# Performance work log

Measured on AMD Instinct MI355X. Metric: run time of the kernel, lower is better.

Reference implementation:

```python
import jax, jax.numpy as jnp
import numpy as np

D_MODEL = 256
D_STATE = 64
D_CONV = 4
EXPAND = 2
HEADDIM = 64
D_INNER = EXPAND * D_MODEL            # 512
NHEADS = D_INNER // HEADDIM           # 8
D_XBC = D_INNER + 2 * D_STATE         # 640 (x, B, C; ngroups=1)
D_IN_PROJ = 2 * D_INNER + 2 * D_STATE + NHEADS  # 1160


def setup_inputs() -> dict:
    key = jax.random.key(0)
    ks = jax.random.split(key, 8)
    x = jax.random.normal(ks[0], (64, 5000, 12), jnp.float32)
    W_in = jax.random.normal(ks[1], (D_MODEL, D_IN_PROJ), jnp.float32) * 0.02
    conv_w = jax.random.normal(ks[2], (D_XBC, D_CONV), jnp.float32) * 0.1
    conv_b = jnp.zeros((D_XBC,), jnp.float32)
    A_log = jnp.log(jax.random.uniform(ks[3], (NHEADS,), jnp.float32, 1.0, 16.0))
    dt_bias = jax.random.normal(ks[4], (NHEADS,), jnp.float32) * 0.1
    D = jnp.ones((NHEADS,), jnp.float32)
    norm_w = jnp.ones((D_INNER,), jnp.float32)
    W_out = jax.random.normal(ks[5], (D_INNER, D_MODEL), jnp.float32) * 0.02
    return {"x": x, "W_in": W_in, "conv_w": conv_w, "conv_b": conv_b,
            "A_log": A_log, "dt_bias": dt_bias, "D": D,
            "norm_w": norm_w, "W_out": W_out}


def _mamba2(u, W_in, conv_w, conv_b, A_log, dt_bias, D, norm_w, W_out):
    b, l, _ = u.shape
    zxbcdt = u @ W_in                                   # (b,l,1160)
    z = zxbcdt[..., :D_INNER]                           # (b,l,512)
    xBC = zxbcdt[..., D_INNER:D_INNER + D_XBC]          # (b,l,640)
    dt = zxbcdt[..., D_INNER + D_XBC:]                  # (b,l,8)
    # causal depthwise conv1d (kernel 4) + SiLU
    xp = jnp.pad(xBC, ((0, 0), (D_CONV - 1, 0), (0, 0)))
    xBC = sum(xp[:, k:k + l, :] * conv_w[:, k] for k in range(D_CONV)) + conv_b
    xBC = jax.nn.silu(xBC)
    xs = xBC[..., :D_INNER].reshape(b, l, NHEADS, HEADDIM)
    Bm = xBC[..., D_INNER:D_INNER + D_STATE]            # (b,l,64)
    Cm = xBC[..., D_INNER + D_STATE:]                   # (b,l,64)
    dt = jax.nn.softplus(dt + dt_bias)                  # (b,l,h)
    A = -jnp.exp(A_log)                                 # (h,)

    def step(h, inp):
        x_t, dt_t, B_t, C_t = inp                       # (b,h,p),(b,h),(b,n),(b,n)
        decay = jnp.exp(dt_t * A)                       # (b,h)
        h = h * decay[..., None, None] + (dt_t[..., None] * x_t)[..., None] * B_t[:, None, None, :]
        y = jnp.einsum('bhpn,bn->bhp', h, C_t)
        return h, y

    h0 = jnp.zeros((b, NHEADS, HEADDIM, D_STATE), u.dtype)
    _, ys = jax.lax.scan(step, h0, (xs.transpose(1, 0, 2, 3), dt.transpose(1, 0, 2),
                                    Bm.transpose(1, 0, 2), Cm.transpose(1, 0, 2)))
    y = ys.transpose(1, 0, 2, 3) + D[None, None, :, None] * xs   # D skip, per head
    y = y.reshape(b, l, D_INNER)
    # RMSNormGated: gate then rmsnorm
    y = y * jax.nn.silu(z)
    y = y * jax.lax.rsqrt(jnp.mean(y * y, axis=-1, keepdims=True) + 1e-5) * norm_w
    return y @ W_out                                    # (b,l,256)


def reference(x, W_in, conv_w, conv_b, A_log, dt_bias, D, norm_w, W_out):
    b = x.shape[0]
    u = x.reshape(b, 250, 240)                          # 'b (t p1) f -> b t (p1 f)'
    u = jnp.pad(u, ((0, 0), (0, 0), (0, D_MODEL - 240)))
    y = _mamba2(u, W_in, conv_w, conv_b, A_log, dt_bias, D, norm_w, W_out)
    y = jax.nn.selu(y)                                  # AlphaDropout is identity at eval
    y = y[..., :240]
    return y.reshape(b, 5000, 12)
```

## Files before the change

kernel.cpp:

```cpp
#include <hip/hip_runtime.h>
#include <cstdint>
#include <cstddef>

#define D_MODEL 256
#define D_STATE 64
#define HEADDIM 64
#define D_INNER 512
#define NHEADS 8
#define D_XBC 640
#define NPROJ 1160
#define ZXW 1152
#define BATCH 64
#define SEQ 250
#define ROWS (BATCH * SEQ)
#define KIN 240
#define KPAD 256
#define NPAD 1280
#define TPAD 256

typedef __bf16 bf16x8 __attribute__((ext_vector_type(8)));
typedef float f32x4 __attribute__((ext_vector_type(4)));

typedef __attribute__((address_space(1))) const void gv_t;
typedef __attribute__((address_space(3))) void lv_t;

__device__ __forceinline__ float readlane_f(float v, int lane) {
    return __uint_as_float(__builtin_amdgcn_readlane(__float_as_uint(v), lane));
}
__device__ __forceinline__ float silu_f(float x) { return x * (1.f / (1.f + __expf(-x))); }
__device__ __forceinline__ unsigned short bf16_rne(float f) {
    unsigned int u = __float_as_uint(f);
    u += 0x7fff + ((u >> 16) & 1);
    return (unsigned short)(u >> 16);
}
__device__ __forceinline__ float bf2f(unsigned short u) {
    return __uint_as_float(((unsigned int)u) << 16);
}
__device__ __forceinline__ unsigned int pack2(float a, float b) {
    return (unsigned int)bf16_rne(a) | ((unsigned int)bf16_rne(b) << 16);
}

#define NA (ROWS * KPAD)
#define NB (NPAD * KPAD)
#define NW (D_MODEL * D_INNER)
__global__ __launch_bounds__(256) void cast_all_kernel(const float* __restrict__ x,
                                                       const float* __restrict__ Win,
                                                       const float* __restrict__ Wout,
                                                       unsigned short* __restrict__ a_bf,
                                                       unsigned short* __restrict__ bt_bf,
                                                       unsigned short* __restrict__ wt_bf) {
    int idx = blockIdx.x * 256 + threadIdx.x;
    if (idx < NA) {
        int row = idx >> 8, c = idx & 255;
        float v = (c < KIN) ? x[row * KIN + c] : 0.f;
        a_bf[idx] = bf16_rne(v);
    } else if (idx < NA + NB) {
        int r = idx - NA;
        int n = r >> 8, k = r & 255;
        float v = (n < NPROJ && k < KIN) ? Win[k * NPROJ + n] : 0.f;
        bt_bf[r] = bf16_rne(v);
    } else if (idx < NA + NB + NW) {
        int r = idx - NA - NB;
        int n = r & 255, k = r >> 8;
        wt_bf[n * D_INNER + k] = bf16_rne(Wout[k * D_MODEL + n]);
    }
}

__global__ __launch_bounds__(256) void gemm1_mfma(const unsigned short* __restrict__ A,
                                                  const unsigned short* __restrict__ Bt,
                                                  unsigned short* __restrict__ Czx,
                                                  float* __restrict__ dtraw) {
    __shared__ unsigned short As[128 * 32];
    __shared__ unsigned short Bs[128 * 32];
    const int tid = threadIdx.x;
    const int lane = tid & 63, wave = tid >> 6;
    const int wm = wave >> 1, wn = wave & 1;
    const int q = lane >> 4, l15 = lane & 15;
    const int rowBase = blockIdx.y * 128, colBase = blockIdx.x * 128;
    f32x4 acc[4][4] = {};

    const int sr = tid >> 2;
    const int sc = (tid & 3) * 8;

    const unsigned short* gA = A + (size_t)(rowBase + sr) * KPAD + sc;
    const unsigned short* gB = Bt + (size_t)(colBase + sr) * KPAD + sc;
    unsigned short* lA = &As[sr * 32 + sc];
    unsigned short* lB = &Bs[sr * 32 + sc];

    for (int k0 = 0; k0 < KPAD; k0 += 32) {
        __builtin_amdgcn_global_load_lds((gv_t*)(gA + k0), (lv_t*)lA, 16, 0, 0);
        __builtin_amdgcn_global_load_lds((gv_t*)(gA + 64 * KPAD + k0),
                                         (lv_t*)(lA + 64 * 32), 16, 0, 0);
        __builtin_amdgcn_global_load_lds((gv_t*)(gB + k0), (lv_t*)lB, 16, 0, 0);
        __builtin_amdgcn_global_load_lds((gv_t*)(gB + 64 * KPAD + k0),
                                         (lv_t*)(lB + 64 * 32), 16, 0, 0);
        __syncthreads();

        bf16x8 bfr[4];
#pragma unroll
        for (int nt = 0; nt < 4; nt++)
            bfr[nt] = *(const bf16x8*)&Bs[(wn * 64 + nt * 16 + l15) * 32 + q * 8];
#pragma unroll
        for (int mt = 0; mt < 4; mt++) {
            bf16x8 afr = *(const bf16x8*)&As[(wm * 64 + mt * 16 + l15) * 32 + q * 8];
#pragma unroll
            for (int nt = 0; nt < 4; nt++)
                acc[mt][nt] = __builtin_amdgcn_mfma_f32_16x16x32_bf16(afr, bfr[nt],
                                                                      acc[mt][nt], 0, 0, 0);
        }
        __syncthreads();
    }
#pragma unroll
    for (int mt = 0; mt < 4; mt++) {
        int grow0 = rowBase + wm * 64 + mt * 16 + q * 4;
#pragma unroll
        for (int nt = 0; nt < 4; nt++) {
            int gcol = colBase + wn * 64 + nt * 16 + l15;
            if (gcol < ZXW) {
#pragma unroll
                for (int reg = 0; reg < 4; reg++) {
                    unsigned int u = bf16_rne(acc[mt][nt][reg]);
                    unsigned int partner = (unsigned int)__shfl_xor((int)u, 1, 64);
                    if ((l15 & 1) == 0)
                        *(unsigned int*)&Czx[(size_t)(grow0 + reg) * ZXW + gcol] =
                            u | (partner << 16);
                }
            } else if (gcol < NPROJ) {
#pragma unroll
                for (int reg = 0; reg < 4; reg++)
                    dtraw[(size_t)(grow0 + reg) * NHEADS + (gcol - ZXW)] = acc[mt][nt][reg];
            }
        }
    }
}

#define CT_IN_STR 68
#define CT_TR_STR 70
__global__ __launch_bounds__(256) void conv_kernel(const unsigned short* __restrict__ zxbc,
                                                   const float* __restrict__ dtraw,
                                                   const float* __restrict__ conv_w,
                                                   const float* __restrict__ conv_b,
                                                   const float* __restrict__ dt_bias,
                                                   unsigned short* __restrict__ xc_bf,
                                                   unsigned short* __restrict__ xcT_bf,
                                                   float* __restrict__ dtp) {
    const int b = blockIdx.x;
    const int t0 = blockIdx.z * 64;
    if (blockIdx.y == 10) {
        for (int it = threadIdx.x; it < 512; it += 256) {
            int h = it & 7;
            int t = t0 + (it >> 3);
            if (t < SEQ) {
                float v = dtraw[(size_t)(b * SEQ + t) * NHEADS + h] + dt_bias[h];
                dtp[(size_t)(b * SEQ + t) * NHEADS + h] =
                    (v > 20.f) ? v : __logf(1.f + __expf(v));
            }
        }
        return;
    }
    __shared__ float In[67 * CT_IN_STR];
    __shared__ unsigned short OutT[64 * CT_TR_STR];
    const int cg = blockIdx.y;
    const int tid = threadIdx.x;
    const int lane = tid & 63;
    const int w = tid >> 6;
    const int ch = cg * 64 + lane;

    for (int r = w; r < 67; r += 4) {
        int t = t0 - 3 + r;
        float v = (t >= 0 && t < SEQ)
                      ? bf2f(zxbc[(size_t)(b * SEQ + t) * ZXW + D_INNER + ch])
                      : 0.f;
        In[r * CT_IN_STR + lane] = v;
    }
    __syncthreads();
    const float w0 = conv_w[ch * 4 + 0], w1 = conv_w[ch * 4 + 1];
    const float w2 = conv_w[ch * 4 + 2], w3 = conv_w[ch * 4 + 3];
    const float bias = conv_b[ch];
    unsigned short vals[16];
#pragma unroll
    for (int i = 0; i < 16; i++) {
        int tt = w * 16 + i;
        float acc = fmaf(w3, In[(tt + 3) * CT_IN_STR + lane],
                    fmaf(w2, In[(tt + 2) * CT_IN_STR + lane],
                    fmaf(w1, In[(tt + 1) * CT_IN_STR + lane],
                    fmaf(w0, In[tt * CT_IN_STR + lane], bias))));
        float sv = silu_f(acc);
        unsigned short bv = (t0 + tt < SEQ) ? bf16_rne(sv) : (unsigned short)0;
        vals[i] = bv;
        OutT[lane * CT_TR_STR + tt] = bv;
    }
#pragma unroll
    for (int i = 0; i < 16; i++) {
        int tt = w * 16 + i;
        if (t0 + tt < SEQ)
            xc_bf[(size_t)(b * SEQ + t0 + tt) * D_XBC + ch] = vals[i];
    }
    __syncthreads();
    unsigned short* dstbase = xcT_bf + ((size_t)b * D_XBC + cg * 64) * TPAD + t0;
#pragma unroll
    for (int i = 0; i < 16; i++) {
        int c2 = w * 16 + i;
        dstbase[(size_t)c2 * TPAD + lane] = OutT[c2 * CT_TR_STR + lane];
    }
}

#define LSTR 72
__global__ __launch_bounds__(256) void scan_intra(const unsigned short* __restrict__ xc_bf,
                                                  const unsigned short* __restrict__ xcT_bf,
                                                  const float* __restrict__ dtp,
                                                  const float* __restrict__ A_log,
                                                  const float* __restrict__ Dvec,
                                                  unsigned short* __restrict__ yout_bf,
                                                  unsigned short* __restrict__ st_g) {
    __shared__ unsigned short C_l[64 * LSTR];
    __shared__ unsigned short BP_l[64 * LSTR];
    __shared__ unsigned short XT_l[64 * LSTR];
    __shared__ float cs_s[64], dts_s[64], fws_s[64];

    const int blk = blockIdx.x;
    const int bh = blk >> 2, c = blk & 3;
    const int b = bh >> 3, h = bh & 7;
    const int tid = threadIdx.x;
    const int lane = tid & 63, w = tid >> 6;
    const int q = lane >> 4, l15 = lane & 15;
    const int t0 = c * 64;
    const float A = -__expf(A_log[h]);
    const float Dh = Dvec[h];

    const int r = tid >> 2, c0 = (tid & 3) * 16;

    {
        if (t0 + r < SEQ) {
            const unsigned short* rowp = xc_bf + (size_t)(b * SEQ + t0 + r) * D_XBC;
            *(uint4*)&C_l[r * LSTR + c0] = *(const uint4*)&rowp[D_INNER + D_STATE + c0];
            *(uint4*)&C_l[r * LSTR + c0 + 8] =
                *(const uint4*)&rowp[D_INNER + D_STATE + c0 + 8];
            *(uint4*)&BP_l[r * LSTR + c0] = *(const uint4*)&rowp[D_INNER + c0];
            *(uint4*)&BP_l[r * LSTR + c0 + 8] = *(const uint4*)&rowp[D_INNER + c0 + 8];
        } else {
            uint4 z = {0, 0, 0, 0};
            *(uint4*)&C_l[r * LSTR + c0] = z;
            *(uint4*)&C_l[r * LSTR + c0 + 8] = z;
            *(uint4*)&BP_l[r * LSTR + c0] = z;
            *(uint4*)&BP_l[r * LSTR + c0 + 8] = z;
        }
        const unsigned short* xrow =
            xcT_bf + ((size_t)b * D_XBC + h * HEADDIM + r) * TPAD + t0;
        *(uint4*)&XT_l[r * LSTR + c0] = *(const uint4*)&xrow[c0];
        *(uint4*)&XT_l[r * LSTR + c0 + 8] = *(const uint4*)&xrow[c0 + 8];
    }
    uint4 braw0, braw1;
    {
        const unsigned short* brow =
            xcT_bf + ((size_t)b * D_XBC + D_INNER + r) * TPAD + t0 + c0;
        braw0 = *(const uint4*)&brow[0];
        braw1 = *(const uint4*)&brow[8];
    }
    if (w == 0) {
        int t = lane;
        float dtv = (t0 + t < SEQ) ? dtp[(size_t)(b * SEQ + t0 + t) * NHEADS + h] : 0.f;
        float csv = dtv * A;
#pragma unroll
        for (int o = 1; o < 64; o <<= 1) {
            float u = __shfl_up(csv, o, 64);
            if (lane >= o) csv += u;
        }
        float tot = readlane_f(csv, 63);
        cs_s[t] = csv;
        dts_s[t] = dtv;
        fws_s[t] = dtv * __expf(tot - csv);
    }
    __syncthreads();

    f32x4 g[4] = {};
#pragma unroll
    for (int k0 = 0; k0 < 64; k0 += 32) {
        bf16x8 ca = *(const bf16x8*)&C_l[(w * 16 + l15) * LSTR + k0 + q * 8];
#pragma unroll
        for (int nt = 0; nt < 4; nt++) {
            bf16x8 bb = *(const bf16x8*)&BP_l[(nt * 16 + l15) * LSTR + k0 + q * 8];
            g[nt] = __builtin_amdgcn_mfma_f32_16x16x32_bf16(ca, bb, g[nt], 0, 0, 0);
        }
    }
    __syncthreads();

    {
        unsigned short tmp[16];
        const unsigned short* rp = (const unsigned short*)&braw0;
#pragma unroll
        for (int j = 0; j < 8; j++) tmp[j] = bf16_rne(bf2f(rp[j]) * fws_s[c0 + j]);
        rp = (const unsigned short*)&braw1;
#pragma unroll
        for (int j = 0; j < 8; j++) tmp[8 + j] = bf16_rne(bf2f(rp[j]) * fws_s[c0 + 8 + j]);
        *(uint4*)&C_l[r * LSTR + c0] = *(uint4*)&tmp[0];
        *(uint4*)&C_l[r * LSTR + c0 + 8] = *(uint4*)&tmp[8];
    }
#pragma unroll
    for (int nt = 0; nt < 4; nt++) {
#pragma unroll
        for (int rr = 0; rr < 4; rr++) {
            int t = w * 16 + q * 4 + rr;
            int s = nt * 16 + l15;
            float pv = 0.f;
            if (s <= t) {
                pv = g[nt][rr] * __expf(cs_s[t] - cs_s[s]) * dts_s[s];
                if (s == t) pv += Dh;
            }
            unsigned int u = bf16_rne(pv);
            unsigned int partner = (unsigned int)__shfl_xor((int)u, 1, 64);
            if ((l15 & 1) == 0)
                *(unsigned int*)&BP_l[t * LSTR + nt * 16 + l15] = u | (partner << 16);
        }
    }
    __syncthreads();

    f32x4 y[4] = {};
#pragma unroll
    for (int k0 = 0; k0 < 64; k0 += 32) {
        bf16x8 pa = *(const bf16x8*)&BP_l[(w * 16 + l15) * LSTR + k0 + q * 8];
#pragma unroll
        for (int nt = 0; nt < 4; nt++) {
            bf16x8 xb = *(const bf16x8*)&XT_l[(nt * 16 + l15) * LSTR + k0 + q * 8];
            y[nt] = __builtin_amdgcn_mfma_f32_16x16x32_bf16(pa, xb, y[nt], 0, 0, 0);
        }
    }
    if (c < 3) {
        f32x4 st[4] = {};
#pragma unroll
        for (int k0 = 0; k0 < 64; k0 += 32) {
            bf16x8 xa = *(const bf16x8*)&XT_l[(w * 16 + l15) * LSTR + k0 + q * 8];
#pragma unroll
            for (int nt = 0; nt < 4; nt++) {
                bf16x8 bwb = *(const bf16x8*)&C_l[(nt * 16 + l15) * LSTR + k0 + q * 8];
                st[nt] = __builtin_amdgcn_mfma_f32_16x16x32_bf16(xa, bwb, st[nt], 0, 0, 0);
            }
        }
        unsigned short* stc = st_g + ((size_t)(bh * 3 + c)) * 4096;
#pragma unroll
        for (int nt = 0; nt < 4; nt++)
#pragma unroll
            for (int rr = 0; rr < 4; rr++) {
                unsigned int u = bf16_rne(st[nt][rr]);
                unsigned int partner = (unsigned int)__shfl_xor((int)u, 1, 64);
                if ((l15 & 1) == 0)
                    *(unsigned int*)&stc[(w * 16 + q * 4 + rr) * 64 + nt * 16 + l15] =
                        u | (partner << 16);
            }
    }
#pragma unroll
    for (int nt = 0; nt < 4; nt++)
#pragma unroll
        for (int rr = 0; rr < 4; rr++) {
            int t = w * 16 + q * 4 + rr;
            if (t0 + t < SEQ) {
                int p = nt * 16 + l15;
                unsigned int u = bf16_rne(y[nt][rr]);
                unsigned int partner = (unsigned int)__shfl_xor((int)u, 1, 64);
                if ((l15 & 1) == 0)
                    *(unsigned int*)&yout_bf[(size_t)(b * SEQ + t0 + t) * D_INNER +
                                             h * HEADDIM + p] = u | (partner << 16);
            }
        }
}

__global__ __launch_bounds__(256) void scan_inter(const unsigned short* __restrict__ xc_bf,
                                                  const float* __restrict__ dtp,
                                                  const float* __restrict__ A_log,
                                                  unsigned short* __restrict__ yout_bf,
                                                  const unsigned short* __restrict__ st_g) {
    __shared__ unsigned short C_l[64 * LSTR];
    __shared__ unsigned short h_l[64 * LSTR];
    __shared__ float cs_s[64];
    __shared__ float csum[4];

    const int blk = blockIdx.x;
    const int bh = blk / 3, c = (blk - bh * 3) + 1;
    const int b = bh >> 3, h = bh & 7;
    const int tid = threadIdx.x;
    const int lane = tid & 63, w = tid >> 6;
    const int q = lane >> 4, l15 = lane & 15;
    const int t0 = c * 64;
    const float A = -__expf(A_log[h]);

    {
        int t = lane;
        int gt = w * 64 + t;
        float dtv = (gt < SEQ) ? dtp[(size_t)(b * SEQ + gt) * NHEADS + h] : 0.f;
        float csv = dtv * A;
#pragma unroll
        for (int o = 1; o < 64; o <<= 1) {
            float u = __shfl_up(csv, o, 64);
            if (lane >= o) csv += u;
        }
        if (w == c) cs_s[t] = csv;
        if (lane == 63) csum[w] = csv;
    }
    {
        int r = tid >> 2, c0 = (tid & 3) * 16;
        if (t0 + r < SEQ) {
            const unsigned short* rowp = xc_bf + (size_t)(b * SEQ + t0 + r) * D_XBC;
            *(uint4*)&C_l[r * LSTR + c0] = *(const uint4*)&rowp[D_INNER + D_STATE + c0];
            *(uint4*)&C_l[r * LSTR + c0 + 8] =
                *(const uint4*)&rowp[D_INNER + D_STATE + c0 + 8];
        } else {
            uint4 z = {0, 0, 0, 0};
            *(uint4*)&C_l[r * LSTR + c0] = z;
            *(uint4*)&C_l[r * LSTR + c0 + 8] = z;
        }
    }
    __syncthreads();

    {
        float wgt[3];
        for (int cp = 0; cp < c; cp++) {
            float s = 0.f;
            for (int j = cp + 1; j < c; j++) s += csum[j];
            wgt[cp] = __expf(s);
        }
        const unsigned short* stb = st_g + (size_t)bh * 3 * 4096;
        for (int i = tid; i < 4096; i += 256) {
            float acc = 0.f;
            for (int cp = 0; cp < c; cp++) acc += wgt[cp] * bf2f(stb[cp * 4096 + i]);
            h_l[(i >> 6) * LSTR + (i & 63)] = bf16_rne(acc);
        }
    }
    __syncthreads();

    f32x4 in[4] = {};
#pragma unroll
    for (int k0 = 0; k0 < 64; k0 += 32) {
        bf16x8 ca = *(const bf16x8*)&C_l[(w * 16 + l15) * LSTR + k0 + q * 8];
#pragma unroll
        for (int nt = 0; nt < 4; nt++) {
            bf16x8 hb = *(const bf16x8*)&h_l[(nt * 16 + l15) * LSTR + k0 + q * 8];
            in[nt] = __builtin_amdgcn_mfma_f32_16x16x32_bf16(ca, hb, in[nt], 0, 0, 0);
        }
    }
#pragma unroll
    for (int nt = 0; nt < 4; nt++)
#pragma unroll
        for (int r = 0; r < 4; r++) {
            int t = w * 16 + q * 4 + r;
            if (t0 + t < SEQ) {
                int p = nt * 16 + l15;
                size_t ai = (size_t)(b * SEQ + t0 + t) * D_INNER + h * HEADDIM + p;
                float alpha = __expf(cs_s[t]);
                float nv = bf2f(yout_bf[ai]) + alpha * in[nt][r];
                unsigned int u = bf16_rne(nv);
                unsigned int partner = (unsigned int)__shfl_xor((int)u, 1, 64);
                if ((l15 & 1) == 0)
                    *(unsigned int*)&yout_bf[ai] = u | (partner << 16);
            }
        }
}

#define SA 40
__global__ __launch_bounds__(256) void gemm2_fused(const unsigned short* __restrict__ yout_bf,
                                                   const unsigned short* __restrict__ zxbc,
                                                   const unsigned short* __restrict__ Bt,
                                                   const float* __restrict__ norm_w,
                                                   float* __restrict__ out) {
    __shared__ unsigned short As2[32 * SA];
    __shared__ unsigned short Bs2[256 * SA];
    __shared__ float rms_s[32];
    const int tid = threadIdx.x;
    const int lane = tid & 63;
    const int wn = tid >> 6;
    const int q = lane >> 4, l15 = lane & 15;
    const int rowBase = blockIdx.x * 32;
    f32x4 acc[2][4] = {};

    const int tr = tid >> 3;
    const int tk = (tid & 7) * 4;

    const unsigned short* yrow = yout_bf + (size_t)(rowBase + tr) * D_INNER + tk;
    const unsigned short* zrow = zxbc + (size_t)(rowBase + tr) * ZXW + tk;
    float ssq = 0.f;

    for (int k0 = 0; k0 < D_INNER; k0 += 32) {
        uint2 yp = *(const uint2*)&yrow[k0];
        uint2 zp = *(const uint2*)&zrow[k0];
        float4 nw = *(const float4*)&norm_w[k0 + tk];
        const unsigned short* ys = (const unsigned short*)&yp;
        const unsigned short* zs = (const unsigned short*)&zp;
        float g0 = bf2f(ys[0]) * silu_f(bf2f(zs[0]));
        float g1 = bf2f(ys[1]) * silu_f(bf2f(zs[1]));
        float g2 = bf2f(ys[2]) * silu_f(bf2f(zs[2]));
        float g3 = bf2f(ys[3]) * silu_f(bf2f(zs[3]));
        ssq = fmaf(g0, g0, ssq);
        ssq = fmaf(g1, g1, ssq);
        ssq = fmaf(g2, g2, ssq);
        ssq = fmaf(g3, g3, ssq);
        uint2 pk;
        pk.x = pack2(g0 * nw.x, g1 * nw.y);
        pk.y = pack2(g2 * nw.z, g3 * nw.w);
        *(uint2*)&As2[tr * SA + tk] = pk;
        const unsigned short* brow = Bt + (size_t)tid * D_INNER + k0;
        *(uint4*)&Bs2[tid * SA + 0] = *(const uint4*)&brow[0];
        *(uint4*)&Bs2[tid * SA + 8] = *(const uint4*)&brow[8];
        *(uint4*)&Bs2[tid * SA + 16] = *(const uint4*)&brow[16];
        *(uint4*)&Bs2[tid * SA + 24] = *(const uint4*)&brow[24];
        __syncthreads();

        bf16x8 bfr[4];
#pragma unroll
        for (int nt = 0; nt < 4; nt++)
            bfr[nt] = *(const bf16x8*)&Bs2[(wn * 64 + nt * 16 + l15) * SA + q * 8];
#pragma unroll
        for (int mt = 0; mt < 2; mt++) {
            bf16x8 afr = *(const bf16x8*)&As2[(mt * 16 + l15) * SA + q * 8];
#pragma unroll
            for (int nt = 0; nt < 4; nt++)
                acc[mt][nt] = __builtin_amdgcn_mfma_f32_16x16x32_bf16(afr, bfr[nt],
                                                                      acc[mt][nt], 0, 0, 0);
        }
        __syncthreads();
    }
    ssq += __shfl_xor(ssq, 1, 64);
    ssq += __shfl_xor(ssq, 2, 64);
    ssq += __shfl_xor(ssq, 4, 64);
    if ((tid & 7) == 0) rms_s[tr] = rsqrtf(ssq * (1.f / 512.f) + 1e-5f);
    __syncthreads();

    const float SC = 1.0507009873554805f, AL = 1.6732632423543772f;
#pragma unroll
    for (int mt = 0; mt < 2; mt++) {
        int lrow0 = mt * 16 + q * 4;
#pragma unroll
        for (int nt = 0; nt < 4; nt++) {
            int gcol = wn * 64 + nt * 16 + l15;
            if (gcol < 240) {
#pragma unroll
                for (int reg = 0; reg < 4; reg++) {
                    float v = acc[mt][nt][reg] * rms_s[lrow0 + reg];
                    v = (v > 0.f) ? SC * v : SC * AL * (__expf(v) - 1.f);
                    out[(size_t)(rowBase + lrow0 + reg) * 240 + gcol] = v;
                }
            }
        }
    }
}

extern "C" void kernel_launch(void* const* d_in, const int* in_sizes, int n_in,
                              void* d_out, int out_size, void* d_ws, size_t ws_size,
                              hipStream_t stream) {
    const float* x = (const float*)d_in[0];
    const float* W_in = (const float*)d_in[1];
    const float* conv_w = (const float*)d_in[2];
    const float* conv_b = (const float*)d_in[3];
    const float* A_log = (const float*)d_in[4];
    const float* dt_bias = (const float*)d_in[5];
    const float* Dv = (const float*)d_in[6];
    const float* norm_w = (const float*)d_in[7];
    const float* W_out = (const float*)d_in[8];
    float* out = (float*)d_out;

    unsigned short* us = (unsigned short*)d_ws;
    unsigned short* zxbc_bf = us;
    unsigned short* xc_bf = zxbc_bf + (size_t)ROWS * ZXW;
    unsigned short* xcT_bf = xc_bf + (size_t)ROWS * D_XBC;
    unsigned short* yout_bf = xcT_bf + (size_t)BATCH * D_XBC * TPAD;
    unsigned short* st_g = yout_bf + (size_t)ROWS * D_INNER;
    unsigned short* bt_bf = st_g + (size_t)512 * 3 * 4096;
    unsigned short* wt_bf = bt_bf + (size_t)NPAD * KPAD;
    float* dtraw = (float*)(wt_bf + (size_t)D_MODEL * D_INNER);
    float* dtp = dtraw + (size_t)ROWS * NHEADS;
    unsigned short* a_bf = (unsigned short*)(dtp + (size_t)ROWS * NHEADS);

    int cast_total = NA + NB + NW;
    cast_all_kernel<<<dim3((cast_total + 255) / 256), 256, 0, stream>>>(x, W_in, W_out,
                                                                        a_bf, bt_bf, wt_bf);

    gemm1_mfma<<<dim3(NPAD / 128, ROWS / 128), 256, 0, stream>>>(a_bf, bt_bf, zxbc_bf, dtraw);

    conv_kernel<<<dim3(BATCH, 11, 4), 256, 0, stream>>>(zxbc_bf, dtraw, conv_w, conv_b,
                                                        dt_bias, xc_bf, xcT_bf, dtp);

    scan_intra<<<dim3(BATCH * NHEADS * 4), 256, 0, stream>>>(xc_bf, xcT_bf, dtp, A_log, Dv,
                                                             yout_bf, st_g);

    scan_inter<<<dim3(BATCH * NHEADS * 3), 256, 0, stream>>>(xc_bf, dtp, A_log,
                                                             yout_bf, st_g);

    gemm2_fused<<<dim3(ROWS / 32), 256, 0, stream>>>(yout_bf, zxbc_bf, wt_bf, norm_w, out);
}
```

Baseline: 205.7 us.

## Fuse intra- and inter-chunk scan into one sequential-chunk kernel per batch-head

Replaces the two scan kernels (intra-chunk, then inter-chunk with states stored to global) with one kernel per (batch, head). It loops over the four chunks in order and carries the running state in registers and LDS, applying the chunk decay each step. This removes the global state buffer traffic, the yout read-modify-write and one launch. The cost is less parallelism: grid drops from 2048 to 512 blocks, each running serially over chunks. The conv kernel also skips redundant row-major and transposed stores for channel groups the scan no longer reads.

Result: faster. 194.5 us (-5.5%).

```diff
diff --git a/kernel.cpp b/kernel.cpp
--- a/kernel.cpp
+++ b/kernel.cpp
@@ -190,47 +190,54 @@
         vals[i] = bv;
         OutT[lane * CT_TR_STR + tt] = bv;
     }
-#pragma unroll
-    for (int i = 0; i < 16; i++) {
-        int tt = w * 16 + i;
-        if (t0 + tt < SEQ)
-            xc_bf[(size_t)(b * SEQ + t0 + tt) * D_XBC + ch] = vals[i];
-    }
-    __syncthreads();
-    unsigned short* dstbase = xcT_bf + ((size_t)b * D_XBC + cg * 64) * TPAD + t0;
-#pragma unroll
-    for (int i = 0; i < 16; i++) {
-        int c2 = w * 16 + i;
-        dstbase[(size_t)c2 * TPAD + lane] = OutT[c2 * CT_TR_STR + lane];
+    if (cg >= 8) {
+#pragma unroll
+        for (int i = 0; i < 16; i++) {
+            int tt = w * 16 + i;
+            if (t0 + tt < SEQ)
+                xc_bf[(size_t)(b * SEQ + t0 + tt) * D_XBC + ch] = vals[i];
+        }
+    }
+    if (cg <= 8) {
+        __syncthreads();
+        unsigned short* dstbase = xcT_bf + ((size_t)b * D_XBC + cg * 64) * TPAD + t0;
+#pragma unroll
+        for (int i = 0; i < 16; i++) {
+            int c2 = w * 16 + i;
+            dstbase[(size_t)c2 * TPAD + lane] = OutT[c2 * CT_TR_STR + lane];
+        }
     }
 }
 
 #define LSTR 72
-__global__ __launch_bounds__(256) void scan_intra(const unsigned short* __restrict__ xc_bf,
+__global__ __launch_bounds__(256) void scan_fused(const unsigned short* __restrict__ xc_bf,
                                                   const unsigned short* __restrict__ xcT_bf,
                                                   const float* __restrict__ dtp,
                                                   const float* __restrict__ A_log,
                                                   const float* __restrict__ Dvec,
-                                                  unsigned short* __restrict__ yout_bf,
-                                                  unsigned short* __restrict__ st_g) {
+                                                  unsigned short* __restrict__ yout_bf) {
     __shared__ unsigned short C_l[64 * LSTR];
     __shared__ unsigned short BP_l[64 * LSTR];
     __shared__ unsigned short XT_l[64 * LSTR];
+    __shared__ unsigned short H_l[64 * LSTR];
     __shared__ float cs_s[64], dts_s[64], fws_s[64];
-
-    const int blk = blockIdx.x;
-    const int bh = blk >> 2, c = blk & 3;
+    __shared__ float tot_s;
+
+    const int bh = blockIdx.x;
     const int b = bh >> 3, h = bh & 7;
     const int tid = threadIdx.x;
     const int lane = tid & 63, w = tid >> 6;
     const int q = lane >> 4, l15 = lane & 15;
-    const int t0 = c * 64;
     const float A = -__expf(A_log[h]);
     const float Dh = Dvec[h];
-
     const int r = tid >> 2, c0 = (tid & 3) * 16;
 
-    {
+    f32x4 h_acc[4] = {};
+
+    for (int c = 0; c < 4; ++c) {
+        const int t0 = c * 64;
+        if (c > 0) __syncthreads();
+
         if (t0 + r < SEQ) {
             const unsigned short* rowp = xc_bf + (size_t)(b * SEQ + t0 + r) * D_XBC;
             *(uint4*)&C_l[r * LSTR + c0] = *(const uint4*)&rowp[D_INNER + D_STATE + c0];
@@ -245,214 +252,138 @@
             *(uint4*)&BP_l[r * LSTR + c0] = z;
             *(uint4*)&BP_l[r * LSTR + c0 + 8] = z;
         }
-        const unsigned short* xrow =
-            xcT_bf + ((size_t)b * D_XBC + h * HEADDIM + r) * TPAD + t0;
-        *(uint4*)&XT_l[r * LSTR + c0] = *(const uint4*)&xrow[c0];
-        *(uint4*)&XT_l[r * LSTR + c0 + 8] = *(const uint4*)&xrow[c0 + 8];
-    }
-    uint4 braw0, braw1;
-    {
-        const unsigned short* brow =
-            xcT_bf + ((size_t)b * D_XBC + D_INNER + r) * TPAD + t0 + c0;
-        braw0 = *(const uint4*)&brow[0];
-        braw1 = *(const uint4*)&brow[8];
-    }
-    if (w == 0) {
-        int t = lane;
-        float dtv = (t0 + t < SEQ) ? dtp[(size_t)(b * SEQ + t0 + t) * NHEADS + h] : 0.f;
-        float csv = dtv * A;
-#pragma unroll
-        for (int o = 1; o < 64; o <<= 1) {
-            float u = __shfl_up(csv, o, 64);
-            if (lane >= o) csv += u;
-        }
-        float tot = readlane_f(csv, 63);
-        cs_s[t] = csv;
-        dts_s[t] = dtv;
-        fws_s[t] = dtv * __expf(tot - csv);
-    }
-    __syncthreads();
-
-    f32x4 g[4] = {};
-#pragma unroll
-    for (int k0 = 0; k0 < 64; k0 += 32) {
-        bf16x8 ca = *(const bf16x8*)&C_l[(w * 16 + l15) * LSTR + k0 + q * 8];
+        {
+            const unsigned short* xrow =
+                xcT_bf + ((size_t)b * D_XBC + h * HEADDIM + r) * TPAD + t0;
+            *(uint4*)&XT_l[r * LSTR + c0] = *(const uint4*)&xrow[c0];
+            *(uint4*)&XT_l[r * LSTR + c0 + 8] = *(const uint4*)&xrow[c0 + 8];
+        }
+        uint4 braw0, braw1;
+        {
+            const unsigned short* brow =
+                xcT_bf + ((size_t)b * D_XBC + D_INNER + r) * TPAD + t0 + c0;
+            braw0 = *(const uint4*)&brow[0];
+            braw1 = *(const uint4*)&brow[8];
+        }
+        if (w == 0) {
+            int t = lane;
+            float dtv = (t0 + t < SEQ) ? dtp[(size_t)(b * SEQ + t0 + t) * NHEADS + h] : 0.f;
+            float csv = dtv * A;
+#pragma unroll
+            for (int o = 1; o < 64; o <<= 1) {
+                float u = __shfl_up(csv, o, 64);
+                if (lane >= o) csv += u;
+            }
+            float tot = readlane_f(csv, 63);
+            cs_s[t] = csv;
+            dts_s[t] = dtv;
+            fws_s[t] = dtv * __expf(tot - csv);
+            if (lane == 0) tot_s = tot;
+        }
+        __syncthreads();
+
+        f32x4 g[4] = {};
+        f32x4 yi[4] = {};
+#pragma unroll
+        for (int k0 = 0; k0 < 64; k0 += 32) {
+            bf16x8 ca = *(const bf16x8*)&C_l[(w * 16 + l15) * LSTR + k0 + q * 8];
+#pragma unroll
+            for (int nt = 0; nt < 4; nt++) {
+                bf16x8 bb = *(const bf16x8*)&BP_l[(nt * 16 + l15) * LSTR + k0 + q * 8];
+                g[nt] = __builtin_amdgcn_mfma_f32_16x16x32_bf16(ca, bb, g[nt], 0, 0, 0);
+            }
+            if (c > 0) {
+#pragma unroll
+                for (int nt = 0; nt < 4; nt++) {
+                    bf16x8 hb = *(const bf16x8*)&H_l[(nt * 16 + l15) * LSTR + k0 + q * 8];
+                    yi[nt] = __builtin_amdgcn_mfma_f32_16x16x32_bf16(ca, hb, yi[nt], 0, 0, 0);
+                }
+            }
+        }
+        __syncthreads();
+
+        {
+            unsigned short tmp[16];
+            const unsigned short* rp = (const unsigned short*)&braw0;
+#pragma unroll
+            for (int j = 0; j < 8; j++) tmp[j] = bf16_rne(bf2f(rp[j]) * fws_s[c0 + j]);
+            rp = (const unsigned short*)&braw1;
+#pragma unroll
+            for (int j = 0; j < 8; j++) tmp[8 + j] = bf16_rne(bf2f(rp[j]) * fws_s[c0 + 8 + j]);
+            *(uint4*)&C_l[r * LSTR + c0] = *(uint4*)&tmp[0];
+            *(uint4*)&C_l[r * LSTR + c0 + 8] = *(uint4*)&tmp[8];
+        }
 #pragma unroll
         for (int nt = 0; nt < 4; nt++) {
-            bf16x8 bb = *(const bf16x8*)&BP_l[(nt * 16 + l15) * LSTR + k0 + q * 8];
-            g[nt] = __builtin_amdgcn_mfma_f32_16x16x32_bf16(ca, bb, g[nt], 0, 0, 0);
-        }
-    }
-    __syncthreads();
-
-    {
-        unsigned short tmp[16];
-        const unsigned short* rp = (const unsigned short*)&braw0;
-#pragma unroll
-        for (int j = 0; j < 8; j++) tmp[j] = bf16_rne(bf2f(rp[j]) * fws_s[c0 + j]);
-        rp = (const unsigned short*)&braw1;
-#pragma unroll
-        for (int j = 0; j < 8; j++) tmp[8 + j] = bf16_rne(bf2f(rp[j]) * fws_s[c0 + 8 + j]);
-        *(uint4*)&C_l[r * LSTR + c0] = *(uint4*)&tmp[0];
-        *(uint4*)&C_l[r * LSTR + c0 + 8] = *(uint4*)&tmp[8];
-    }
-#pragma unroll
-    for (int nt = 0; nt < 4; nt++) {
-#pragma unroll
-        for (int rr = 0; rr < 4; rr++) {
-            int t = w * 16 + q * 4 + rr;
-            int s = nt * 16 + l15;
-            float pv = 0.f;
-            if (s <= t) {
-                pv = g[nt][rr] * __expf(cs_s[t] - cs_s[s]) * dts_s[s];
-                if (s == t) pv += Dh;
-            }
-            unsigned int u = bf16_rne(pv);
-            unsigned int partner = (unsigned int)__shfl_xor((int)u, 1, 64);
-            if ((l15 & 1) == 0)
-                *(unsigned int*)&BP_l[t * LSTR + nt * 16 + l15] = u | (partner << 16);
-        }
-    }
-    __syncthreads();
-
-    f32x4 y[4] = {};
-#pragma unroll
-    for (int k0 = 0; k0 < 64; k0 += 32) {
-        bf16x8 pa = *(const bf16x8*)&BP_l[(w * 16 + l15) * LSTR + k0 + q * 8];
-#pragma unroll
-        for (int nt = 0; nt < 4; nt++) {
-            bf16x8 xb = *(const bf16x8*)&XT_l[(nt * 16 + l15) * LSTR + k0 + q * 8];
-            y[nt] = __builtin_amdgcn_mfma_f32_16x16x32_bf16(pa, xb, y[nt], 0, 0, 0);
-        }
-    }
-    if (c < 3) {
-        f32x4 st[4] = {};
-#pragma unroll
-        for (int k0 = 0; k0 < 64; k0 += 32) {
-            bf16x8 xa = *(const bf16x8*)&XT_l[(w * 16 + l15) * LSTR + k0 + q * 8];
-#pragma unroll
-            for (int nt = 0; nt < 4; nt++) {
-                bf16x8 bwb = *(const bf16x8*)&C_l[(nt * 16 + l15) * LSTR + k0 + q * 8];
-                st[nt] = __builtin_amdgcn_mfma_f32_16x16x32_bf16(xa, bwb, st[nt], 0, 0, 0);
-            }
-        }
-        unsigned short* stc = st_g + ((size_t)(bh * 3 + c)) * 4096;
-#pragma unroll
-        for (int nt = 0; nt < 4; nt++)
 #pragma unroll
             for (int rr = 0; rr < 4; rr++) {
-                unsigned int u = bf16_rne(st[nt][rr]);
+                int t = w * 16 + q * 4 + rr;
+                int s = nt * 16 + l15;
+                float pv = 0.f;
+                if (s <= t) {
+                    pv = g[nt][rr] * __expf(cs_s[t] - cs_s[s]) * dts_s[s];
+                    if (s == t) pv += Dh;
+                }
+                unsigned int u = bf16_rne(pv);
                 unsigned int partner = (unsigned int)__shfl_xor((int)u, 1, 64);
                 if ((l15 & 1) == 0)
-                    *(unsigned int*)&stc[(w * 16 + q * 4 + rr) * 64 + nt * 16 + l15] =
-                        u | (partner << 16);
-            }
-    }
-#pragma unroll
-    for (int nt = 0; nt < 4; nt++)
-#pragma unroll
-        for (int rr = 0; rr < 4; rr++) {
-            int t = w * 16 + q * 4 + rr;
-            if (t0 + t < SEQ) {
-                int p = nt * 16 + l15;
-                unsigned int u = bf16_rne(y[nt][rr]);
-                unsigned int partner = (unsigned int)__shfl_xor((int)u, 1, 64);
-                if ((l15 & 1) == 0)
-                    *(unsigned int*)&yout_bf[(size_t)(b * SEQ + t0 + t) * D_INNER +
-                                             h * HEADDIM + p] = u | (partner << 16);
-            }
-        }
-}
-
-__global__ __launch_bounds__(256) void scan_inter(const unsigned short* __restrict__ xc_bf,
-                                                  const float* __restrict__ dtp,
-                                                  const float* __restrict__ A_log,
-                                                  unsigned short* __restrict__ yout_bf,
-                                                  const unsigned short* __restrict__ st_g) {
-    __shared__ unsigned short C_l[64 * LSTR];
-    __shared__ unsigned short h_l[64 * LSTR];
-    __shared__ float cs_s[64];
-    __shared__ float csum[4];
-
-    const int blk = blockIdx.x;
-    const int bh = blk / 3, c = (blk - bh * 3) + 1;
-    const int b = bh >> 3, h = bh & 7;
-    const int tid = threadIdx.x;
-    const int lane = tid & 63, w = tid >> 6;
-    const int q = lane >> 4, l15 = lane & 15;
-    const int t0 = c * 64;
-    const float A = -__expf(A_log[h]);
-
-    {
-        int t = lane;
-        int gt = w * 64 + t;
-        float dtv = (gt < SEQ) ? dtp[(size_t)(b * SEQ + gt) * NHEADS + h] : 0.f;
-        float csv = dtv * A;
-#pragma unroll
-        for (int o = 1; o < 64; o <<= 1) {
-            float u = __shfl_up(csv, o, 64);
-            if (lane >= o) csv += u;
-        }
-        if (w == c) cs_s[t] = csv;
-        if (lane == 63) csum[w] = csv;
-    }
-    {
-        int r = tid >> 2, c0 = (tid & 3) * 16;
-        if (t0 + r < SEQ) {
-            const unsigned short* rowp = xc_bf + (size_t)(b * SEQ + t0 + r) * D_XBC;
-            *(uint4*)&C_l[r * LSTR + c0] = *(const uint4*)&rowp[D_INNER + D_STATE + c0];
-            *(uint4*)&C_l[r * LSTR + c0 + 8] =
-                *(const uint4*)&rowp[D_INNER + D_STATE + c0 + 8];
-        } else {
-            uint4 z = {0, 0, 0, 0};
-            *(uint4*)&C_l[r * LSTR + c0] = z;
-            *(uint4*)&C_l[r * LSTR + c0 + 8] = z;
-        }
-    }
-    __syncthreads();
-
-    {
-        float wgt[3];
-        for (int cp = 0; cp < c; cp++) {
-            float s = 0.f;
-            for (int j = cp + 1; j < c; j++) s += csum[j];
-            wgt[cp] = __expf(s);
-        }
-        const unsigned short* stb = st_g + (size_t)bh * 3 * 4096;
-        for (int i = tid; i < 4096; i += 256) {
-            float acc = 0.f;
-            for (int cp = 0; cp < c; cp++) acc += wgt[cp] * bf2f(stb[cp * 4096 + i]);
-            h_l[(i >> 6) * LSTR + (i & 63)] = bf16_rne(acc);
-        }
-    }
-    __syncthreads();
-
-    f32x4 in[4] = {};
-#pragma unroll
-    for (int k0 = 0; k0 < 64; k0 += 32) {
-        bf16x8 ca = *(const bf16x8*)&C_l[(w * 16 + l15) * LSTR + k0 + q * 8];
-#pragma unroll
-        for (int nt = 0; nt < 4; nt++) {
-            bf16x8 hb = *(const bf16x8*)&h_l[(nt * 16 + l15) * LSTR + k0 + q * 8];
-            in[nt] = __builtin_amdgcn_mfma_f32_16x16x32_bf16(ca, hb, in[nt], 0, 0, 0);
-        }
-    }
-#pragma unroll
-    for (int nt = 0; nt < 4; nt++)
-#pragma unroll
-        for (int r = 0; r < 4; r++) {
-            int t = w * 16 + q * 4 + r;
-            if (t0 + t < SEQ) {
-                int p = nt * 16 + l15;
-                size_t ai = (size_t)(b * SEQ + t0 + t) * D_INNER + h * HEADDIM + p;
-                float alpha = __expf(cs_s[t]);
-                float nv = bf2f(yout_bf[ai]) + alpha * in[nt][r];
-                unsigned int u = bf16_rne(nv);
-                unsigned int partner = (unsigned int)__shfl_xor((int)u, 1, 64);
-                if ((l15 & 1) == 0)
-                    *(unsigned int*)&yout_bf[ai] = u | (partner << 16);
-            }
-        }
+                    *(unsigned int*)&BP_l[t * LSTR + nt * 16 + l15] = u | (partner << 16);
+            }
+        }
+        __syncthreads();
+
+        f32x4 y[4] = {};
+#pragma unroll
+        for (int k0 = 0; k0 < 64; k0 += 32) {
+            bf16x8 pa = *(const bf16x8*)&BP_l[(w * 16 + l15) * LSTR + k0 + q * 8];
+#pragma unroll
+            for (int nt = 0; nt < 4; nt++) {
+                bf16x8 xb = *(const bf16x8*)&XT_l[(nt * 16 + l15) * LSTR + k0 + q * 8];
+                y[nt] = __builtin_amdgcn_mfma_f32_16x16x32_bf16(pa, xb, y[nt], 0, 0, 0);
+            }
+        }
+        if (c < 3) {
+            f32x4 st[4] = {};
+#pragma unroll
+            for (int k0 = 0; k0 < 64; k0 += 32) {
+                bf16x8 xa = *(const bf16x8*)&XT_l[(w * 16 + l15) * LSTR + k0 + q * 8];
+#pragma unroll
+                for (int nt = 0; nt < 4; nt++) {
+                    bf16x8 bwb = *(const bf16x8*)&C_l[(nt * 16 + l15) * LSTR + k0 + q * 8];
+                    st[nt] = __builtin_amdgcn_mfma_f32_16x16x32_bf16(xa, bwb, st[nt], 0, 0, 0);
+                }
+            }
+            const float decay = __expf(tot_s);
+#pragma unroll
+            for (int nt = 0; nt < 4; nt++) {
+                h_acc[nt] = st[nt] + decay * h_acc[nt];
+#pragma unroll
+                for (int rr = 0; rr < 4; rr++) {
+                    unsigned int u = bf16_rne(h_acc[nt][rr]);
+                    unsigned int partner = (unsigned int)__shfl_xor((int)u, 1, 64);
+                    if ((l15 & 1) == 0)
+                        *(unsigned int*)&H_l[(w * 16 + q * 4 + rr) * LSTR + nt * 16 + l15] =
+                            u | (partner << 16);
+                }
+            }
+        }
+#pragma unroll
+        for (int nt = 0; nt < 4; nt++)
+#pragma unroll
+            for (int rr = 0; rr < 4; rr++) {
+                int t = w * 16 + q * 4 + rr;
+                if (t0 + t < SEQ) {
+                    int p = nt * 16 + l15;
+                    float yv = y[nt][rr];
+                    if (c > 0) yv += __expf(cs_s[t]) * yi[nt][rr];
+                    unsigned int u = bf16_rne(yv);
+                    unsigned int partner = (unsigned int)__shfl_xor((int)u, 1, 64);
+                    if ((l15 & 1) == 0)
+                        *(unsigned int*)&yout_bf[(size_t)(b * SEQ + t0 + t) * D_INNER +
+                                                 h * HEADDIM + p] = u | (partner << 16);
+                }
+            }
+    }
 }
 
 #define SA 40
@@ -577,11 +508,8 @@
     conv_kernel<<<dim3(BATCH, 11, 4), 256, 0, stream>>>(zxbc_bf, dtraw, conv_w, conv_b,
                                                         dt_bias, xc_bf, xcT_bf, dtp);
 
-    scan_intra<<<dim3(BATCH * NHEADS * 4), 256, 0, stream>>>(xc_bf, xcT_bf, dtp, A_log, Dv,
-                                                             yout_bf, st_g);
-
-    scan_inter<<<dim3(BATCH * NHEADS * 3), 256, 0, stream>>>(xc_bf, dtp, A_log,
-                                                             yout_bf, st_g);
+    scan_fused<<<dim3(BATCH * NHEADS), 256, 0, stream>>>(xc_bf, xcT_bf, dtp, A_log, Dv,
+                                                         yout_bf);
 
     gemm2_fused<<<dim3(ROWS / 32), 256, 0, stream>>>(yout_bf, zxbc_bf, wt_bf, norm_w, out);
 }
```
